# Optimization experiments

Hardware: AMD Instinct MI355X
Metric: run time of the kernel (lower is better)

Reference implementation:

```python
import jax, jax.numpy as jnp
import numpy as np

N_NODES, N_EDGES = 50000, 800000
NODE_DIM, EDGE_DIM, HIDDEN, NUM_LAYERS = 64, 32, 64, 2
IN_MSG = NODE_DIM + EDGE_DIM  # 96
IN_UPD = NODE_DIM + HIDDEN    # 128


def setup_inputs() -> dict:
    key = jax.random.key(0)
    ks = jax.random.split(key, 12)
    def w(k, shape, fan_in):
        return jax.random.normal(k, shape, jnp.float32) * (1.0 / np.sqrt(fan_in))
    return {
        "node_features": jax.random.normal(ks[0], (N_NODES, NODE_DIM), jnp.float32),
        "edge_features": jax.random.normal(ks[1], (N_EDGES, EDGE_DIM), jnp.float32),
        "msg_w1": w(ks[2], (NUM_LAYERS, IN_MSG, HIDDEN), IN_MSG),
        "msg_b1": w(ks[3], (NUM_LAYERS, HIDDEN), IN_MSG),
        "msg_w2": w(ks[4], (NUM_LAYERS, HIDDEN, HIDDEN), HIDDEN),
        "msg_b2": w(ks[5], (NUM_LAYERS, HIDDEN), HIDDEN),
        "upd_w1": w(ks[6], (IN_UPD, HIDDEN), IN_UPD),
        "upd_b1": w(ks[7], (HIDDEN,), IN_UPD),
        "upd_w2": w(ks[8], (HIDDEN, NODE_DIM), HIDDEN),
        "upd_b2": w(ks[9], (NODE_DIM,), HIDDEN),
        "src": jax.random.randint(ks[10], (N_EDGES,), 0, N_NODES, dtype=jnp.int32),
        "dst": jax.random.randint(ks[11], (N_EDGES,), 0, N_NODES, dtype=jnp.int32),
    }


def reference(node_features, edge_features, msg_w1, msg_b1, msg_w2, msg_b2,
              upd_w1, upd_b1, upd_w2, upd_b2, src, dst):
    n_nodes = node_features.shape[0]
    # message: concat gathered source node feats with edge feats -> [E, node+edge]
    combined = jnp.concatenate([node_features[src], edge_features], axis=-1)
    # sum over the num_layers small Linear-ReLU-Linear message networks
    msg = jnp.zeros((combined.shape[0], msg_w2.shape[-1]), combined.dtype)
    for l in range(msg_w1.shape[0]):  # small fixed num_layers
        h = jax.nn.relu(combined @ msg_w1[l] + msg_b1[l])
        msg = msg + (h @ msg_w2[l] + msg_b2[l])
    # scatter-sum messages to destination nodes, normalize by neighbor count
    agg = jax.ops.segment_sum(msg, dst, num_segments=n_nodes)
    deg = jax.ops.segment_sum(jnp.ones((dst.shape[0],), msg.dtype), dst, num_segments=n_nodes)
    agg = agg / (deg[:, None] + 1e-8)
    # update MLP on concat(node, aggregated)
    comb2 = jnp.concatenate([node_features, agg], axis=-1)
    return jax.nn.relu(comb2 @ upd_w1 + upd_b1) @ upd_w2 + upd_b2
```

## Files before the change

### kernel.cpp

```cpp
#include <hip/hip_runtime.h>

#define NN 50000
#define NE 800000
#define ND 64
#define ED 32
#define HID 64
#define NL 2
#define IN_MSG 96
#define IN_UPD 128

#define W1_LD 104
#define MSG_LD 72
#define UPD_LD 136

#define NBLK 512
#define WPB 4
#define TOTW (NBLK * WPB)
#define NGRP (NE / 32)
#define NB_SCAN 196

typedef __attribute__((ext_vector_type(8))) short short8;
typedef __attribute__((ext_vector_type(4))) float f32x4;

__device__ inline ushort bf16r(float f) {
    union { float f; unsigned u; } x; x.f = f;
    return (ushort)((x.u + 0x7FFFu + ((x.u >> 16) & 1u)) >> 16);
}
__device__ inline float b2f(unsigned u) {
    union { unsigned u; float f; } x; x.u = u << 16; return x.f;
}
__device__ inline short8 pk8(float4 a, float4 b) {
    short8 r;
    r[0] = (short)bf16r(a.x); r[1] = (short)bf16r(a.y);
    r[2] = (short)bf16r(a.z); r[3] = (short)bf16r(a.w);
    r[4] = (short)bf16r(b.x); r[5] = (short)bf16r(b.y);
    r[6] = (short)bf16r(b.z); r[7] = (short)bf16r(b.w);
    return r;
}
__device__ inline uint2 pack4(float4 v) {
    return make_uint2((unsigned)bf16r(v.x) | ((unsigned)bf16r(v.y) << 16),
                      (unsigned)bf16r(v.z) | ((unsigned)bf16r(v.w) << 16));
}

__global__ __launch_bounds__(256) void hist_kernel(const int* __restrict__ dst,
                                                   int* __restrict__ cnt)
{
    const int i = blockIdx.x * 256 + threadIdx.x;
    atomicAdd(&cnt[dst[i]], 1);
}

__global__ __launch_bounds__(256) void scanA_kernel(const int* __restrict__ cnt,
                                                    int* __restrict__ off,
                                                    int* __restrict__ bsum)
{
    __shared__ int buf[256];
    const int t = threadIdx.x;
    const int i = blockIdx.x * 256 + t;
    const int v = (i < NN) ? cnt[i] : 0;
    buf[t] = v;
    __syncthreads();
    #pragma unroll
    for (int d = 1; d < 256; d <<= 1) {
        const int x = (t >= d) ? buf[t - d] : 0;
        __syncthreads();
        buf[t] += x;
        __syncthreads();
    }
    if (i < NN) off[i] = buf[t] - v;
    if (t == 255) bsum[blockIdx.x] = buf[255];
}

__global__ __launch_bounds__(256) void scanB_kernel(int* __restrict__ bsum)
{
    __shared__ int buf[256];
    const int t = threadIdx.x;
    buf[t] = (t < NB_SCAN) ? bsum[t] : 0;
    __syncthreads();
    #pragma unroll
    for (int d = 1; d < 256; d <<= 1) {
        const int x = (t >= d) ? buf[t - d] : 0;
        __syncthreads();
        buf[t] += x;
        __syncthreads();
    }
    if (t < NB_SCAN) bsum[t] = buf[t];
}

__global__ __launch_bounds__(256) void scanC_kernel(const int* __restrict__ bsum,
                                                    int* __restrict__ off,
                                                    int* __restrict__ cursor)
{
    const int b = blockIdx.x;
    const int i = b * 256 + threadIdx.x;
    const int boff = (b > 0) ? bsum[b - 1] : 0;
    if (i < NN) {
        const int e = off[i] + boff;
        off[i] = e;
        cursor[i] = e;
    }
    if (i == 0) off[NN] = NE;
}

__global__ __launch_bounds__(256) void fill_kernel(const int* __restrict__ src,
                                                   const int* __restrict__ dst,
                                                   int* __restrict__ cursor,
                                                   int* __restrict__ esort,
                                                   int* __restrict__ ssort,
                                                   int* __restrict__ dsort)
{
    const int i = blockIdx.x * 256 + threadIdx.x;
    const int d = dst[i];
    const int pos = atomicAdd(&cursor[d], 1);
    esort[pos] = i;
    ssort[pos] = src[i];
    dsort[pos] = d;
}

template <int SORTED>
__global__ __launch_bounds__(256, 2)
void msg_kernel(const float* __restrict__ nf,
                const float* __restrict__ ef,
                const float* __restrict__ w1,
                const float* __restrict__ b1,
                const float* __restrict__ w2,
                const float* __restrict__ b2,
                const int* __restrict__ src,
                const int* __restrict__ dst,
                const int* __restrict__ esort,
                const int* __restrict__ ssort,
                const int* __restrict__ dsort,
                float* __restrict__ agg,
                float* __restrict__ deg)
{
    __shared__ __align__(16) ushort sW1t[NL][64][W1_LD];
    __shared__ __align__(16) ushort sW2t[NL][64][64];
    __shared__ __align__(16) ushort sMS[WPB][32][MSG_LD];

    const int tid = threadIdx.x;
    const int w  = tid >> 6;
    const int l  = tid & 63;
    const int lr = l & 15;
    const int lg = l >> 4;

    {
        const int k16 = tid >> 4, n0 = (tid & 15) * 4;
        #pragma unroll
        for (int lay = 0; lay < NL; ++lay) {
            #pragma unroll
            for (int it = 0; it < 6; ++it) {
                const int k = k16 + 16 * it;
                const float4 v = *reinterpret_cast<const float4*>(
                    w1 + ((size_t)lay * IN_MSG + k) * HID + n0);
                sW1t[lay][n0 + 0][k] = bf16r(v.x);
                sW1t[lay][n0 + 1][k] = bf16r(v.y);
                sW1t[lay][n0 + 2][k] = bf16r(v.z);
                sW1t[lay][n0 + 3][k] = bf16r(v.w);
            }
            #pragma unroll
            for (int it = 0; it < 4; ++it) {
                const int k = k16 + 16 * it;
                const float4 v = *reinterpret_cast<const float4*>(
                    w2 + ((size_t)lay * HID + k) * HID + n0);
                const ushort vals[4] = {bf16r(v.x), bf16r(v.y), bf16r(v.z), bf16r(v.w)};
                #pragma unroll
                for (int j = 0; j < 4; ++j) {
                    const int row = n0 + j;
                    const int colS = (((k >> 3) ^ (row & 7)) << 3) | (k & 7);
                    sW2t[lay][row][colS] = vals[j];
                }
            }
        }
    }
    float bias1[NL][4], bias2s[4];
    #pragma unroll
    for (int lay = 0; lay < NL; ++lay)
        #pragma unroll
        for (int nt = 0; nt < 4; ++nt)
            bias1[lay][nt] = b1[lay * HID + nt * 16 + lr];
    #pragma unroll
    for (int nt = 0; nt < 4; ++nt)
        bias2s[nt] = b2[nt * 16 + lr] + b2[HID + nt * 16 + lr];
    __syncthreads();

    const float4* nfr = reinterpret_cast<const float4*>(nf);
    const float4* efr = reinterpret_cast<const float4*>(ef);

    int g = blockIdx.x * WPB + w;
    int ev = 0, sv = 0, dv = 0;
    int en = 0, sn = 0, dn = 0;
    if (l < 32) {
        if (SORTED) { ev = esort[(size_t)g * 32 + l]; sv = ssort[(size_t)g * 32 + l];
                      dv = dsort[(size_t)g * 32 + l]; }
        else        { sv = src[(size_t)g * 32 + l];   dv = dst[(size_t)g * 32 + l]; }
    }
    {
        const int gn = g + TOTW;
        if (gn < NGRP && l < 32) {
            if (SORTED) { en = esort[(size_t)gn * 32 + l]; sn = ssort[(size_t)gn * 32 + l];
                          dn = dsort[(size_t)gn * 32 + l]; }
            else        { sn = src[(size_t)gn * 32 + l];   dn = dst[(size_t)gn * 32 + l]; }
        }
    }
    float4 nfv[2][4], efv[2][2];
    #pragma unroll
    for (int mt = 0; mt < 2; ++mt) {
        const int s = __shfl(sv, mt * 16 + lr);
        const float4* p = nfr + (size_t)s * 16;
        nfv[mt][0] = p[2 * lg];     nfv[mt][1] = p[2 * lg + 1];
        nfv[mt][2] = p[8 + 2 * lg]; nfv[mt][3] = p[9 + 2 * lg];
        const int e = SORTED ? __shfl(ev, mt * 16 + lr) : (g * 32 + mt * 16 + lr);
        const float4* q = efr + (size_t)e * 8;
        efv[mt][0] = q[2 * lg];
        efv[mt][1] = q[2 * lg + 1];
    }

    #pragma unroll 1
    while (g < NGRP) {
        const int gn  = g + TOTW;
        const int gnn = g + 2 * TOTW;
        const bool more = (gn < NGRP);

        short8 cmbA[2][3];
        #pragma unroll
        for (int mt = 0; mt < 2; ++mt) {
            cmbA[mt][0] = pk8(nfv[mt][0], nfv[mt][1]);
            cmbA[mt][1] = pk8(nfv[mt][2], nfv[mt][3]);
            cmbA[mt][2] = pk8(efv[mt][0], efv[mt][1]);
        }

        int en2 = 0, sn2 = 0, dn2 = 0;
        if (gnn < NGRP && l < 32) {
            if (SORTED) { en2 = esort[(size_t)gnn * 32 + l]; sn2 = ssort[(size_t)gnn * 32 + l];
                          dn2 = dsort[(size_t)gnn * 32 + l]; }
            else        { sn2 = src[(size_t)gnn * 32 + l];   dn2 = dst[(size_t)gnn * 32 + l]; }
        }
        float4 nfn[2][4], efn[2][2];
        if (more) {
            #pragma unroll
            for (int mt = 0; mt < 2; ++mt) {
                const int e = SORTED ? __shfl(en, mt * 16 + lr) : (gn * 32 + mt * 16 + lr);
                const float4* q = efr + (size_t)e * 8;
                efn[mt][0] = q[2 * lg];
                efn[mt][1] = q[2 * lg + 1];
                const int s = __shfl(sn, mt * 16 + lr);
                const float4* p = nfr + (size_t)s * 16;
                nfn[mt][0] = p[2 * lg];     nfn[mt][1] = p[2 * lg + 1];
                nfn[mt][2] = p[8 + 2 * lg]; nfn[mt][3] = p[9 + 2 * lg];
            }
        }

        f32x4 msg[2][4];
        #pragma unroll
        for (int nt = 0; nt < 4; ++nt) {
            const float v = bias2s[nt];
            msg[0][nt] = (f32x4){v, v, v, v};
            msg[1][nt] = (f32x4){v, v, v, v};
        }

        #pragma unroll
        for (int lay = 0; lay < NL; ++lay) {
            #pragma unroll
            for (int mt = 0; mt < 2; ++mt) {
                f32x4 acc[4];
                #pragma unroll
                for (int nt = 0; nt < 4; ++nt) {
                    const float bv = bias1[lay][nt];
                    acc[nt] = (f32x4){bv, bv, bv, bv};
                }
                __builtin_amdgcn_s_setprio(1);
                #pragma unroll
                for (int ks = 0; ks < 3; ++ks)
                    #pragma unroll
                    for (int nt = 0; nt < 4; ++nt) {
                        const short8 B = *reinterpret_cast<const short8*>(
                            &sW1t[lay][nt * 16 + lr][ks * 32 + 8 * lg]);
                        acc[nt] = __builtin_amdgcn_mfma_f32_16x16x32_bf16(
                            cmbA[mt][ks], B, acc[nt], 0, 0, 0);
                    }
                __builtin_amdgcn_s_setprio(0);
                #pragma unroll
                for (int nt = 0; nt < 4; ++nt)
                    #pragma unroll
                    for (int r = 0; r < 4; ++r)
                        sMS[w][4 * lg + r][nt * 16 + lr] = bf16r(fmaxf(acc[nt][r], 0.0f));
                const short8 h0 = *reinterpret_cast<const short8*>(&sMS[w][lr][ 0 + 8 * lg]);
                const short8 h1 = *reinterpret_cast<const short8*>(&sMS[w][lr][32 + 8 * lg]);
                __builtin_amdgcn_s_setprio(1);
                #pragma unroll
                for (int nt = 0; nt < 4; ++nt) {
                    const int cB = nt * 16 + lr;
                    const short8 B0 = *reinterpret_cast<const short8*>(
                        &sW2t[lay][cB][((0 + lg) ^ (lr & 7)) << 3]);
                    const short8 B1 = *reinterpret_cast<const short8*>(
                        &sW2t[lay][cB][((4 + lg) ^ (lr & 7)) << 3]);
                    msg[mt][nt] = __builtin_amdgcn_mfma_f32_16x16x32_bf16(h0, B0, msg[mt][nt], 0, 0, 0);
                    msg[mt][nt] = __builtin_amdgcn_mfma_f32_16x16x32_bf16(h1, B1, msg[mt][nt], 0, 0, 0);
                }
                __builtin_amdgcn_s_setprio(0);
            }
        }

        if (SORTED) {
            #pragma unroll
            for (int mt = 0; mt < 2; ++mt)
                #pragma unroll
                for (int nt = 0; nt < 4; ++nt)
                    #pragma unroll
                    for (int r = 0; r < 4; ++r)
                        sMS[w][mt * 16 + 4 * lg + r][nt * 16 + lr] = bf16r(msg[mt][nt][r]);
            {
                float acc = 0.0f;
                #pragma unroll
                for (int r = 0; r < 32; ++r) {
                    acc += b2f((unsigned)sMS[w][r][l]);
                    const int dr = __shfl(dv, r);
                    const bool cut = (r == 31) || (dr != __shfl(dv, r + 1));
                    if (cut) {
                        atomicAdd(&agg[(size_t)dr * HID + l], acc);
                        acc = 0.0f;
                    }
                }
            }
        } else {
            #pragma unroll
            for (int mt = 0; mt < 2; ++mt)
                #pragma unroll
                for (int r = 0; r < 4; ++r) {
                    const int drow = __shfl(dv, mt * 16 + 4 * lg + r);
                    float* rowp = agg + (size_t)drow * HID;
                    #pragma unroll
                    for (int nt = 0; nt < 4; ++nt)
                        atomicAdd(rowp + nt * 16 + lr, msg[mt][nt][r]);
                }
            if (l < 32) atomicAdd(&deg[dv], 1.0f);
        }

        ev = en; sv = sn; dv = dn;
        en = en2; sn = sn2; dn = dn2;
        #pragma unroll
        for (int mt = 0; mt < 2; ++mt) {
            #pragma unroll
            for (int i = 0; i < 4; ++i) nfv[mt][i] = nfn[mt][i];
            efv[mt][0] = efn[mt][0]; efv[mt][1] = efn[mt][1];
        }
        g = gn;
    }
}

template <int USE_OFF>
__global__ __launch_bounds__(256, 2)
void node_update_kernel(const float* __restrict__ nf,
                        const float* __restrict__ agg,
                        const int* __restrict__ off,
                        const float* __restrict__ degf,
                        const float* __restrict__ uw1,
                        const float* __restrict__ ub1,
                        const float* __restrict__ uw2,
                        const float* __restrict__ ub2,
                        float* __restrict__ out)
{
    __shared__ __align__(16) ushort sAct[WPB][32][UPD_LD];
    __shared__ __align__(16) ushort sW1t[64][UPD_LD];
    __shared__ __align__(16) ushort sW2t[64][MSG_LD];
    __shared__ float sUB1[64], sUB2[64];

    const int tid = threadIdx.x;
    const int w  = tid >> 6;
    const int l  = tid & 63;
    const int lr = l & 15;
    const int lg = l >> 4;

    {
        const int k16 = tid >> 4, n0 = (tid & 15) * 4;
        #pragma unroll
        for (int it = 0; it < 8; ++it) {
            const int k = k16 + 16 * it;
            const float4 v = *reinterpret_cast<const float4*>(uw1 + (size_t)k * HID + n0);
            sW1t[n0 + 0][k] = bf16r(v.x);
            sW1t[n0 + 1][k] = bf16r(v.y);
            sW1t[n0 + 2][k] = bf16r(v.z);
            sW1t[n0 + 3][k] = bf16r(v.w);
        }
        #pragma unroll
        for (int it = 0; it < 4; ++it) {
            const int k = k16 + 16 * it;
            const float4 v = *reinterpret_cast<const float4*>(uw2 + (size_t)k * ND + n0);
            sW2t[n0 + 0][k] = bf16r(v.x);
            sW2t[n0 + 1][k] = bf16r(v.y);
            sW2t[n0 + 2][k] = bf16r(v.z);
            sW2t[n0 + 3][k] = bf16r(v.w);
        }
        if (tid < 64) { sUB1[tid] = ub1[tid]; sUB2[tid] = ub2[tid]; }
    }

    const int nbase = blockIdx.x * 128 + w * 32;
    float invv = 0.0f;
    if (l < 32) {
        const int n = min(nbase + l, NN - 1);
        const float d = USE_OFF ? (float)(off[n + 1] - off[n]) : degf[n];
        invv = 1.0f / (d + 1e-8f);
    }

    #pragma unroll
    for (int it = 0; it < 8; ++it) {
        const int row = lg + 4 * it;
        const int n = min(nbase + row, NN - 1);
        const float4 v = reinterpret_cast<const float4*>(nf + (size_t)n * ND)[lr];
        *reinterpret_cast<uint2*>(&sAct[w][row][lr * 4]) = pack4(v);
    }
    #pragma unroll
    for (int it = 0; it < 8; ++it) {
        const int row = lg + 4 * it;
        const int n = min(nbase + row, NN - 1);
        const float iv = __shfl(invv, row);
        float4 v = reinterpret_cast<const float4*>(agg + (size_t)n * HID)[lr];
        v.x *= iv; v.y *= iv; v.z *= iv; v.w *= iv;
        *reinterpret_cast<uint2*>(&sAct[w][row][ND + lr * 4]) = pack4(v);
    }
    __syncthreads();

    short8 A[2][4];
    #pragma unroll
    for (int mt = 0; mt < 2; ++mt)
        #pragma unroll
        for (int ks = 0; ks < 4; ++ks)
            A[mt][ks] = *reinterpret_cast<const short8*>(&sAct[w][mt * 16 + lr][ks * 32 + 8 * lg]);
    #pragma unroll
    for (int nt = 0; nt < 4; ++nt) {
        const int cB = nt * 16 + lr;
        short8 B[4];
        #pragma unroll
        for (int ks = 0; ks < 4; ++ks)
            B[ks] = *reinterpret_cast<const short8*>(&sW1t[cB][ks * 32 + 8 * lg]);
        const float bv = sUB1[cB];
        #pragma unroll
        for (int mt = 0; mt < 2; ++mt) {
            f32x4 acc = (f32x4){bv, bv, bv, bv};
            #pragma unroll
            for (int ks = 0; ks < 4; ++ks)
                acc = __builtin_amdgcn_mfma_f32_16x16x32_bf16(A[mt][ks], B[ks], acc, 0, 0, 0);
            const int rH = mt * 16 + 4 * lg;
            #pragma unroll
            for (int r = 0; r < 4; ++r)
                sAct[w][rH + r][cB] = bf16r(fmaxf(acc[r], 0.0f));
        }
    }

    f32x4 o[2][4];
    #pragma unroll
    for (int nt = 0; nt < 4; ++nt) {
        const float v = sUB2[nt * 16 + lr];
        o[0][nt] = (f32x4){v, v, v, v};
        o[1][nt] = (f32x4){v, v, v, v};
    }
    #pragma unroll
    for (int mt = 0; mt < 2; ++mt) {
        const short8 A0 = *reinterpret_cast<const short8*>(&sAct[w][mt * 16 + lr][ 0 + 8 * lg]);
        const short8 A1 = *reinterpret_cast<const short8*>(&sAct[w][mt * 16 + lr][32 + 8 * lg]);
        #pragma unroll
        for (int nt = 0; nt < 4; ++nt) {
            const int cB = nt * 16 + lr;
            const short8 B0 = *reinterpret_cast<const short8*>(&sW2t[cB][ 0 + 8 * lg]);
            const short8 B1 = *reinterpret_cast<const short8*>(&sW2t[cB][32 + 8 * lg]);
            o[mt][nt] = __builtin_amdgcn_mfma_f32_16x16x32_bf16(A0, B0, o[mt][nt], 0, 0, 0);
            o[mt][nt] = __builtin_amdgcn_mfma_f32_16x16x32_bf16(A1, B1, o[mt][nt], 0, 0, 0);
        }
    }

    #pragma unroll
    for (int mt = 0; mt < 2; ++mt)
        #pragma unroll
        for (int r = 0; r < 4; ++r) {
            const int n = nbase + mt * 16 + 4 * lg + r;
            if (n < NN) {
                float* rowp = out + (size_t)n * ND;
                #pragma unroll
                for (int nt = 0; nt < 4; ++nt)
                    rowp[nt * 16 + lr] = o[mt][nt][r];
            }
        }
}

extern "C" void kernel_launch(void* const* d_in, const int* in_sizes, int n_in,
                              void* d_out, int out_size, void* d_ws, size_t ws_size,
                              hipStream_t stream)
{
    const float* nf  = (const float*)d_in[0];
    const float* ef  = (const float*)d_in[1];
    const float* w1  = (const float*)d_in[2];
    const float* b1  = (const float*)d_in[3];
    const float* w2  = (const float*)d_in[4];
    const float* b2  = (const float*)d_in[5];
    const float* uw1 = (const float*)d_in[6];
    const float* ub1 = (const float*)d_in[7];
    const float* uw2 = (const float*)d_in[8];
    const float* ub2 = (const float*)d_in[9];
    const int*   src = (const int*)d_in[10];
    const int*   dst = (const int*)d_in[11];
    float* out = (float*)d_out;

    constexpr size_t ESB  = (size_t)NE * 4;
    constexpr size_t SSB  = (size_t)NE * 4;
    constexpr size_t DSB  = (size_t)NE * 4;
    constexpr size_t OFFB = (size_t)(NN + 1) * 4 + 12;
    constexpr size_t CNTB = (size_t)NN * 4;
    constexpr size_t BSUMB = 1024;
    constexpr size_t AGGB = (size_t)NN * HID * 4;
    constexpr size_t NEED = ESB + SSB + DSB + OFFB + CNTB + BSUMB + AGGB;

    if (ws_size >= NEED) {
        char* p = (char*)d_ws;
        int* esort = (int*)p;              p += ESB;
        int* ssort = (int*)p;              p += SSB;
        int* dsort = (int*)p;              p += DSB;
        int* off   = (int*)p;              p += OFFB;
        int* cnt   = (int*)p;              p += CNTB;
        int* bsum  = (int*)p;              p += BSUMB;
        float* agg = (float*)p;

        (void)hipMemsetAsync(cnt, 0, CNTB, stream);
        (void)hipMemsetAsync(agg, 0, AGGB, stream);
        hist_kernel<<<NE / 256, 256, 0, stream>>>(dst, cnt);
        scanA_kernel<<<NB_SCAN, 256, 0, stream>>>(cnt, off, bsum);
        scanB_kernel<<<1, 256, 0, stream>>>(bsum);
        scanC_kernel<<<NB_SCAN, 256, 0, stream>>>(bsum, off, cnt);
        fill_kernel<<<NE / 256, 256, 0, stream>>>(src, dst, cnt, esort, ssort, dsort);
        msg_kernel<1><<<NBLK, 256, 0, stream>>>(nf, ef, w1, b1, w2, b2, src, dst,
                                                esort, ssort, dsort, agg, nullptr);
        node_update_kernel<1><<<(NN + 127) / 128, 256, 0, stream>>>(
            nf, agg, off, nullptr, uw1, ub1, uw2, ub2, out);
    } else {
        float* agg = (float*)d_ws;
        float* deg = agg + (size_t)NN * HID;
        (void)hipMemsetAsync(d_ws, 0, ((size_t)NN * HID + NN) * sizeof(float), stream);
        msg_kernel<0><<<NBLK, 256, 0, stream>>>(nf, ef, w1, b1, w2, b2, src, dst,
                                                nullptr, nullptr, nullptr, agg, deg);
        node_update_kernel<0><<<(NN + 127) / 128, 256, 0, stream>>>(
            nf, agg, nullptr, deg, uw1, ub1, uw2, ub2, out);
    }
}
```

Measured before the change: 208.9 us.

## Keep W2 fragments in registers, swap MFMA operands, pack sorted edge indices

The second-layer weights now live in registers as MFMA fragments instead of a swizzled LDS tile, and both message-network GEMMs are computed transposed (weights as the A operand) so results can be written to LDS as packed 4-wide bf16 stores. The two row tiles are processed together per layer, biases come from LDS, and the scatter loop uses readlane instead of shuffles. Sorted edge id, source and destination are packed into one int4 array so a single load fetches all three. This aims to cut LDS traffic and the number of index loads, at the cost of more VGPRs (64 extra registers for W2 fragments) and a larger index buffer with one padding word per edge.

```diff
diff --git a/kernel.cpp b/kernel.cpp
--- a/kernel.cpp
+++ b/kernel.cpp
@@ -41,6 +41,10 @@
     return make_uint2((unsigned)bf16r(v.x) | ((unsigned)bf16r(v.y) << 16),
                       (unsigned)bf16r(v.z) | ((unsigned)bf16r(v.w) << 16));
 }
+__device__ inline uint2 pkacc(f32x4 a) {
+    return make_uint2((unsigned)bf16r(a[0]) | ((unsigned)bf16r(a[1]) << 16),
+                      (unsigned)bf16r(a[2]) | ((unsigned)bf16r(a[3]) << 16));
+}
 
 __global__ __launch_bounds__(256) void hist_kernel(const int* __restrict__ dst,
                                                    int* __restrict__ cnt)
@@ -104,16 +108,12 @@
 __global__ __launch_bounds__(256) void fill_kernel(const int* __restrict__ src,
                                                    const int* __restrict__ dst,
                                                    int* __restrict__ cursor,
-                                                   int* __restrict__ esort,
-                                                   int* __restrict__ ssort,
-                                                   int* __restrict__ dsort)
+                                                   int4* __restrict__ esd)
 {
     const int i = blockIdx.x * 256 + threadIdx.x;
     const int d = dst[i];
     const int pos = atomicAdd(&cursor[d], 1);
-    esort[pos] = i;
-    ssort[pos] = src[i];
-    dsort[pos] = d;
+    esd[pos] = make_int4(i, src[i], d, 0);
 }
 
 template <int SORTED>
@@ -126,15 +126,14 @@
                 const float* __restrict__ b2,
                 const int* __restrict__ src,
                 const int* __restrict__ dst,
-                const int* __restrict__ esort,
-                const int* __restrict__ ssort,
-                const int* __restrict__ dsort,
+                const int4* __restrict__ esd,
                 float* __restrict__ agg,
                 float* __restrict__ deg)
 {
     __shared__ __align__(16) ushort sW1t[NL][64][W1_LD];
-    __shared__ __align__(16) ushort sW2t[NL][64][64];
     __shared__ __align__(16) ushort sMS[WPB][32][MSG_LD];
+    __shared__ __align__(16) float sB1f[NL][64];
+    __shared__ __align__(16) float sB2f[64];
 
     const int tid = threadIdx.x;
     const int w  = tid >> 6;
@@ -145,7 +144,7 @@
     {
         const int k16 = tid >> 4, n0 = (tid & 15) * 4;
         #pragma unroll
-        for (int lay = 0; lay < NL; ++lay) {
+        for (int lay = 0; lay < NL; ++lay)
             #pragma unroll
             for (int it = 0; it < 6; ++it) {
                 const int k = k16 + 16 * it;
@@ -156,30 +155,23 @@
                 sW1t[lay][n0 + 2][k] = bf16r(v.z);
                 sW1t[lay][n0 + 3][k] = bf16r(v.w);
             }
-            #pragma unroll
-            for (int it = 0; it < 4; ++it) {
-                const int k = k16 + 16 * it;
-                const float4 v = *reinterpret_cast<const float4*>(
-                    w2 + ((size_t)lay * HID + k) * HID + n0);
-                const ushort vals[4] = {bf16r(v.x), bf16r(v.y), bf16r(v.z), bf16r(v.w)};
+        if (tid < NL * 64) sB1f[tid >> 6][tid & 63] = b1[tid];
+        if (tid < 64) sB2f[tid] = b2[tid] + b2[HID + tid];
+    }
+    short8 w2f[NL][4][2];
+    #pragma unroll
+    for (int lay = 0; lay < NL; ++lay)
+        #pragma unroll
+        for (int nt = 0; nt < 4; ++nt)
+            #pragma unroll
+            for (int ks = 0; ks < 2; ++ks) {
+                short8 t;
                 #pragma unroll
-                for (int j = 0; j < 4; ++j) {
-                    const int row = n0 + j;
-                    const int colS = (((k >> 3) ^ (row & 7)) << 3) | (k & 7);
-                    sW2t[lay][row][colS] = vals[j];
-                }
-            }
-        }
-    }
-    float bias1[NL][4], bias2s[4];
-    #pragma unroll
-    for (int lay = 0; lay < NL; ++lay)
-        #pragma unroll
-        for (int nt = 0; nt < 4; ++nt)
-            bias1[lay][nt] = b1[lay * HID + nt * 16 + lr];
-    #pragma unroll
-    for (int nt = 0; nt < 4; ++nt)
-        bias2s[nt] = b2[nt * 16 + lr] + b2[HID + nt * 16 + lr];
+                for (int j = 0; j < 8; ++j)
+                    t[j] = (short)bf16r(
+                        w2[((size_t)lay * HID + ks * 32 + 8 * lg + j) * HID + nt * 16 + lr]);
+                w2f[lay][nt][ks] = t;
+            }
     __syncthreads();
 
     const float4* nfr = reinterpret_cast<const float4*>(nf);
@@ -189,16 +181,14 @@
     int ev = 0, sv = 0, dv = 0;
     int en = 0, sn = 0, dn = 0;
     if (l < 32) {
-        if (SORTED) { ev = esort[(size_t)g * 32 + l]; sv = ssort[(size_t)g * 32 + l];
-                      dv = dsort[(size_t)g * 32 + l]; }
-        else        { sv = src[(size_t)g * 32 + l];   dv = dst[(size_t)g * 32 + l]; }
+        if (SORTED) { const int4 t = esd[(size_t)g * 32 + l]; ev = t.x; sv = t.y; dv = t.z; }
+        else        { sv = src[(size_t)g * 32 + l]; dv = dst[(size_t)g * 32 + l]; }
     }
     {
         const int gn = g + TOTW;
         if (gn < NGRP && l < 32) {
-            if (SORTED) { en = esort[(size_t)gn * 32 + l]; sn = ssort[(size_t)gn * 32 + l];
-                          dn = dsort[(size_t)gn * 32 + l]; }
-            else        { sn = src[(size_t)gn * 32 + l];   dn = dst[(size_t)gn * 32 + l]; }
+            if (SORTED) { const int4 t = esd[(size_t)gn * 32 + l]; en = t.x; sn = t.y; dn = t.z; }
+            else        { sn = src[(size_t)gn * 32 + l]; dn = dst[(size_t)gn * 32 + l]; }
         }
     }
     float4 nfv[2][4], efv[2][2];
@@ -230,9 +220,8 @@
 
         int en2 = 0, sn2 = 0, dn2 = 0;
         if (gnn < NGRP && l < 32) {
-            if (SORTED) { en2 = esort[(size_t)gnn * 32 + l]; sn2 = ssort[(size_t)gnn * 32 + l];
-                          dn2 = dsort[(size_t)gnn * 32 + l]; }
-            else        { sn2 = src[(size_t)gnn * 32 + l];   dn2 = dst[(size_t)gnn * 32 + l]; }
+            if (SORTED) { const int4 t = esd[(size_t)gnn * 32 + l]; en2 = t.x; sn2 = t.y; dn2 = t.z; }
+            else        { sn2 = src[(size_t)gnn * 32 + l]; dn2 = dst[(size_t)gnn * 32 + l]; }
         }
         float4 nfn[2][4], efn[2][2];
         if (more) {
@@ -252,86 +241,83 @@
         f32x4 msg[2][4];
         #pragma unroll
         for (int nt = 0; nt < 4; ++nt) {
-            const float v = bias2s[nt];
-            msg[0][nt] = (f32x4){v, v, v, v};
-            msg[1][nt] = (f32x4){v, v, v, v};
+            const f32x4 b2v = *reinterpret_cast<const f32x4*>(&sB2f[nt * 16 + 4 * lg]);
+            msg[0][nt] = b2v;
+            msg[1][nt] = b2v;
         }
 
         #pragma unroll
         for (int lay = 0; lay < NL; ++lay) {
-            #pragma unroll
-            for (int mt = 0; mt < 2; ++mt) {
-                f32x4 acc[4];
+            f32x4 acc[2][4];
+            #pragma unroll
+            for (int nt = 0; nt < 4; ++nt) {
+                const f32x4 bv = *reinterpret_cast<const f32x4*>(&sB1f[lay][nt * 16 + 4 * lg]);
+                acc[0][nt] = bv;
+                acc[1][nt] = bv;
+            }
+            __builtin_amdgcn_s_setprio(1);
+            #pragma unroll
+            for (int ks = 0; ks < 3; ++ks)
                 #pragma unroll
                 for (int nt = 0; nt < 4; ++nt) {
-                    const float bv = bias1[lay][nt];
-                    acc[nt] = (f32x4){bv, bv, bv, bv};
+                    const short8 Bw = *reinterpret_cast<const short8*>(
+                        &sW1t[lay][nt * 16 + lr][ks * 32 + 8 * lg]);
+                    acc[0][nt] = __builtin_amdgcn_mfma_f32_16x16x32_bf16(Bw, cmbA[0][ks], acc[0][nt], 0, 0, 0);
+                    acc[1][nt] = __builtin_amdgcn_mfma_f32_16x16x32_bf16(Bw, cmbA[1][ks], acc[1][nt], 0, 0, 0);
                 }
-                __builtin_amdgcn_s_setprio(1);
-                #pragma unroll
-                for (int ks = 0; ks < 3; ++ks)
-                    #pragma unroll
-                    for (int nt = 0; nt < 4; ++nt) {
-                        const short8 B = *reinterpret_cast<const short8*>(
-                            &sW1t[lay][nt * 16 + lr][ks * 32 + 8 * lg]);
-                        acc[nt] = __builtin_amdgcn_mfma_f32_16x16x32_bf16(
-                            cmbA[mt][ks], B, acc[nt], 0, 0, 0);
-                    }
-                __builtin_amdgcn_s_setprio(0);
-                #pragma unroll
-                for (int nt = 0; nt < 4; ++nt)
-                    #pragma unroll
-                    for (int r = 0; r < 4; ++r)
-                        sMS[w][4 * lg + r][nt * 16 + lr] = bf16r(fmaxf(acc[nt][r], 0.0f));
-                const short8 h0 = *reinterpret_cast<const short8*>(&sMS[w][lr][ 0 + 8 * lg]);
-                const short8 h1 = *reinterpret_cast<const short8*>(&sMS[w][lr][32 + 8 * lg]);
-                __builtin_amdgcn_s_setprio(1);
+            __builtin_amdgcn_s_setprio(0);
+            #pragma unroll
+            for (int mt = 0; mt < 2; ++mt)
                 #pragma unroll
                 for (int nt = 0; nt < 4; ++nt) {
-                    const int cB = nt * 16 + lr;
-                    const short8 B0 = *reinterpret_cast<const short8*>(
-                        &sW2t[lay][cB][((0 + lg) ^ (lr & 7)) << 3]);
-                    const short8 B1 = *reinterpret_cast<const short8*>(
-                        &sW2t[lay][cB][((4 + lg) ^ (lr & 7)) << 3]);
-                    msg[mt][nt] = __builtin_amdgcn_mfma_f32_16x16x32_bf16(h0, B0, msg[mt][nt], 0, 0, 0);
-                    msg[mt][nt] = __builtin_amdgcn_mfma_f32_16x16x32_bf16(h1, B1, msg[mt][nt], 0, 0, 0);
+                    f32x4 a = acc[mt][nt];
+                    a[0] = fmaxf(a[0], 0.0f); a[1] = fmaxf(a[1], 0.0f);
+                    a[2] = fmaxf(a[2], 0.0f); a[3] = fmaxf(a[3], 0.0f);
+                    *reinterpret_cast<uint2*>(&sMS[w][mt * 16 + lr][nt * 16 + 4 * lg]) = pkacc(a);
                 }
-                __builtin_amdgcn_s_setprio(0);
-            }
-        }
-
-        if (SORTED) {
+            short8 hA[2][2];
             #pragma unroll
             for (int mt = 0; mt < 2; ++mt)
                 #pragma unroll
-                for (int nt = 0; nt < 4; ++nt)
-                    #pragma unroll
-                    for (int r = 0; r < 4; ++r)
-                        sMS[w][mt * 16 + 4 * lg + r][nt * 16 + lr] = bf16r(msg[mt][nt][r]);
-            {
-                float acc = 0.0f;
+                for (int ks = 0; ks < 2; ++ks)
+                    hA[mt][ks] = *reinterpret_cast<const short8*>(
+                        &sMS[w][mt * 16 + lr][ks * 32 + 8 * lg]);
+            __builtin_amdgcn_s_setprio(1);
+            #pragma unroll
+            for (int ks = 0; ks < 2; ++ks)
                 #pragma unroll
-                for (int r = 0; r < 32; ++r) {
-                    acc += b2f((unsigned)sMS[w][r][l]);
-                    const int dr = __shfl(dv, r);
-                    const bool cut = (r == 31) || (dr != __shfl(dv, r + 1));
-                    if (cut) {
-                        atomicAdd(&agg[(size_t)dr * HID + l], acc);
-                        acc = 0.0f;
-                    }
+                for (int nt = 0; nt < 4; ++nt) {
+                    msg[0][nt] = __builtin_amdgcn_mfma_f32_16x16x32_bf16(w2f[lay][nt][ks], hA[0][ks], msg[0][nt], 0, 0, 0);
+                    msg[1][nt] = __builtin_amdgcn_mfma_f32_16x16x32_bf16(w2f[lay][nt][ks], hA[1][ks], msg[1][nt], 0, 0, 0);
                 }
+            __builtin_amdgcn_s_setprio(0);
+        }
+
+        #pragma unroll
+        for (int mt = 0; mt < 2; ++mt)
+            #pragma unroll
+            for (int nt = 0; nt < 4; ++nt)
+                *reinterpret_cast<uint2*>(&sMS[w][mt * 16 + lr][nt * 16 + 4 * lg]) = pkacc(msg[mt][nt]);
+
+        if (SORTED) {
+            float acc = 0.0f;
+            int dr = __builtin_amdgcn_readlane(dv, 0);
+            #pragma unroll
+            for (int r = 0; r < 32; ++r) {
+                acc += b2f((unsigned)sMS[w][r][l]);
+                const int drn = (r < 31) ? __builtin_amdgcn_readlane(dv, r + 1) : -1;
+                if (r == 31 || dr != drn) {
+                    atomicAdd(&agg[(size_t)dr * HID + l], acc);
+                    acc = 0.0f;
+                }
+                dr = drn;
             }
         } else {
             #pragma unroll
-            for (int mt = 0; mt < 2; ++mt)
-                #pragma unroll
-                for (int r = 0; r < 4; ++r) {
-                    const int drow = __shfl(dv, mt * 16 + 4 * lg + r);
-                    float* rowp = agg + (size_t)drow * HID;
-                    #pragma unroll
-                    for (int nt = 0; nt < 4; ++nt)
-                        atomicAdd(rowp + nt * 16 + lr, msg[mt][nt][r]);
-                }
+            for (int r = 0; r < 32; ++r) {
+                const int dr = __builtin_amdgcn_readlane(dv, r);
+                atomicAdd(&agg[(size_t)dr * HID + l], b2f((unsigned)sMS[w][r][l]));
+            }
             if (l < 32) atomicAdd(&deg[dv], 1.0f);
         }
 
@@ -499,23 +485,19 @@
     const int*   dst = (const int*)d_in[11];
     float* out = (float*)d_out;
 
-    constexpr size_t ESB  = (size_t)NE * 4;
-    constexpr size_t SSB  = (size_t)NE * 4;
-    constexpr size_t DSB  = (size_t)NE * 4;
+    constexpr size_t ESDB = (size_t)NE * 16;
     constexpr size_t OFFB = (size_t)(NN + 1) * 4 + 12;
     constexpr size_t CNTB = (size_t)NN * 4;
     constexpr size_t BSUMB = 1024;
     constexpr size_t AGGB = (size_t)NN * HID * 4;
-    constexpr size_t NEED = ESB + SSB + DSB + OFFB + CNTB + BSUMB + AGGB;
+    constexpr size_t NEED = ESDB + OFFB + CNTB + BSUMB + AGGB;
 
     if (ws_size >= NEED) {
         char* p = (char*)d_ws;
-        int* esort = (int*)p;              p += ESB;
-        int* ssort = (int*)p;              p += SSB;
-        int* dsort = (int*)p;              p += DSB;
-        int* off   = (int*)p;              p += OFFB;
-        int* cnt   = (int*)p;              p += CNTB;
-        int* bsum  = (int*)p;              p += BSUMB;
+        int4* esd  = (int4*)p;             p += ESDB;
+        int*  off  = (int*)p;              p += OFFB;
+        int*  cnt  = (int*)p;              p += CNTB;
+        int*  bsum = (int*)p;              p += BSUMB;
         float* agg = (float*)p;
 
         (void)hipMemsetAsync(cnt, 0, CNTB, stream);
@@ -524,9 +506,9 @@
         scanA_kernel<<<NB_SCAN, 256, 0, stream>>>(cnt, off, bsum);
         scanB_kernel<<<1, 256, 0, stream>>>(bsum);
         scanC_kernel<<<NB_SCAN, 256, 0, stream>>>(bsum, off, cnt);
-        fill_kernel<<<NE / 256, 256, 0, stream>>>(src, dst, cnt, esort, ssort, dsort);
+        fill_kernel<<<NE / 256, 256, 0, stream>>>(src, dst, cnt, esd);
         msg_kernel<1><<<NBLK, 256, 0, stream>>>(nf, ef, w1, b1, w2, b2, src, dst,
-                                                esort, ssort, dsort, agg, nullptr);
+                                                esd, agg, nullptr);
         node_update_kernel<1><<<(NN + 127) / 128, 256, 0, stream>>>(
             nf, agg, off, nullptr, uw1, ub1, uw2, ub2, out);
     } else {
@@ -534,7 +516,7 @@
         float* deg = agg + (size_t)NN * HID;
         (void)hipMemsetAsync(d_ws, 0, ((size_t)NN * HID + NN) * sizeof(float), stream);
         msg_kernel<0><<<NBLK, 256, 0, stream>>>(nf, ef, w1, b1, w2, b2, src, dst,
-                                                nullptr, nullptr, nullptr, agg, deg);
+                                                nullptr, agg, deg);
         node_update_kernel<0><<<(NN + 127) / 128, 256, 0, stream>>>(
             nf, agg, nullptr, deg, uw1, ub1, uw2, ub2, out);
     }
```

New measurement: 203.1 us. 1.03x faster.
